# Kernel tuning notes

Hardware: AMD Instinct MI355X
Metric: run time of the kernel (lower is better)

The kernel has to match this reference:

```python
import jax, jax.numpy as jnp
import numpy as np

N_PER_GRAPH = 1000   # nodes per graph block (shape of A)
N_GRAPHS = 100       # number of block-diagonal replicas
N = N_PER_GRAPH * N_GRAPHS  # total nodes = 100000
HIDDEN = 128
DEG = 8
E = N * DEG          # total edges = 800000
LN_EPS = 1e-5


def setup_inputs() -> dict:
    key = jax.random.key(0)
    kx, kr, kc, kw, kb = jax.random.split(key, 5)
    # x rows: [S(N); I(N); R(N); params(N)] with beta in col0, gamma in col1
    x = jax.random.normal(kx, (4 * N, HIDDEN), dtype=jnp.float32)
    # block-diagonal COO edges: indices within each graph offset by graph id * n
    offs = jnp.repeat(jnp.arange(N_GRAPHS, dtype=jnp.int64) * N_PER_GRAPH,
                      N_PER_GRAPH * DEG)
    edge_row = offs + jax.random.randint(kr, (E,), 0, N_PER_GRAPH, dtype=jnp.int64)
    edge_col = offs + jax.random.randint(kc, (E,), 0, N_PER_GRAPH, dtype=jnp.int64)
    W = jax.random.normal(kw, (HIDDEN, HIDDEN), dtype=jnp.float32)
    b = jax.random.normal(kb, (HIDDEN,), dtype=jnp.float32)
    ln_w = jnp.ones((HIDDEN,), dtype=jnp.float32)
    ln_b = jnp.zeros((HIDDEN,), dtype=jnp.float32)
    t = jax.random.uniform(jax.random.fold_in(key, 7), (1,), dtype=jnp.float32)
    return {"t": t, "x": x, "edge_row": edge_row, "edge_col": edge_col,
            "W": W, "b": b, "ln_w": ln_w, "ln_b": ln_b}


def reference(t, x, edge_row, edge_col, W, b, ln_w, ln_b):
    n4 = x.shape[0]
    n = n4 // 4
    sir = x[: 3 * n]                       # [3N, H]
    beta = x[3 * n :, 0]                   # [N]
    gam = x[3 * n :, 1]                    # [N]
    h = jax.nn.relu(sir @ W.T + b)         # Linear + ReLU
    S, I, R = h[:n], h[n : 2 * n], h[2 * n :]
    # block-diagonal adjacency aggregation: AI[row] += I[col]
    AI = jax.ops.segment_sum(I[edge_col], edge_row, num_segments=n)
    dS = -beta[:, None] * (AI * S)
    dI = -dS - gam[:, None] * I
    dR = gam[:, None] * I

    def ln(v):
        m = jnp.mean(v, axis=-1, keepdims=True)
        var = jnp.mean(jnp.square(v - m), axis=-1, keepdims=True)
        return (v - m) * jax.lax.rsqrt(var + LN_EPS) * ln_w + ln_b

    return jnp.concatenate([ln(dS), ln(dI), ln(dR), x[3 * n :]], axis=0)
```

## Files before the change

kernel.cpp:

```cpp
#include <hip/hip_runtime.h>

#define HID 128
#define NPG 1000
#define NGRAPH 100
#define NNODES (NPG * NGRAPH)
#define DEG 8
#define LN_EPS 1e-5f

#define K1_ROWS 128

typedef _Float16 half8 __attribute__((ext_vector_type(8)));
typedef float f32x4 __attribute__((ext_vector_type(4)));

__device__ inline void cvt_split(const float4 a, const float4 b,
                                 half8& hi, half8& lo)
{
    float v[8] = {a.x, a.y, a.z, a.w, b.x, b.y, b.z, b.w};
    #pragma unroll
    for (int i = 0; i < 8; ++i) {
        _Float16 h = (_Float16)v[i];
        hi[i] = h;
        lo[i] = (_Float16)(v[i] - (float)h);
    }
}

__global__ __launch_bounds__(256, 2) void k_gemm_relu(
    const float* __restrict__ x, const float* __restrict__ W,
    const float* __restrict__ bias, float* __restrict__ outS,
    float* __restrict__ outI, int nrows)
{
    __shared__ alignas(16) _Float16 Xh[K1_ROWS * 64];
    __shared__ alignas(16) _Float16 Xl[K1_ROWS * 64];
    __shared__ alignas(16) _Float16 Wh[HID * 64];
    __shared__ alignas(16) _Float16 Wl[HID * 64];

    const int tid  = threadIdx.x;
    const int lane = tid & 63;
    const int w    = tid >> 6;
    const int wr   = (w >> 1) * 64;
    const int wc   = (w & 1) * 64;
    const int r0   = blockIdx.x * K1_ROWS;

    f32x4 acc[4][4];
    #pragma unroll
    for (int i = 0; i < 4; ++i)
        #pragma unroll
        for (int j = 0; j < 4; ++j)
            acc[i][j] = (f32x4){0.f, 0.f, 0.f, 0.f};

    const int l15 = lane & 15;
    const int lg  = lane >> 4;
    const int swz = (lane & 7) << 3;

    for (int kh = 0; kh < 2; ++kh) {
        if (kh) __syncthreads();

        #pragma unroll
        for (int it = 0; it < 4; ++it) {
            int chunk = tid + it * 256;
            int row = chunk >> 3, kg = chunk & 7;
            const float* gp = &x[(size_t)(r0 + row) * HID + kh * 64 + kg * 8];
            float4 a = reinterpret_cast<const float4*>(gp)[0];
            float4 b = reinterpret_cast<const float4*>(gp)[1];
            half8 hi, lo; cvt_split(a, b, hi, lo);
            int widx = (row * 64 + kg * 8) ^ ((row & 7) << 3);
            *reinterpret_cast<half8*>(&Xh[widx]) = hi;
            *reinterpret_cast<half8*>(&Xl[widx]) = lo;
        }
        #pragma unroll
        for (int it = 0; it < 4; ++it) {
            int chunk = tid + it * 256;
            int row = chunk >> 3, kg = chunk & 7;
            const float* gp = &W[(size_t)row * HID + kh * 64 + kg * 8];
            float4 a = reinterpret_cast<const float4*>(gp)[0];
            float4 b = reinterpret_cast<const float4*>(gp)[1];
            half8 hi, lo; cvt_split(a, b, hi, lo);
            int widx = (row * 64 + kg * 8) ^ ((row & 7) << 3);
            *reinterpret_cast<half8*>(&Wh[widx]) = hi;
            *reinterpret_cast<half8*>(&Wl[widx]) = lo;
        }
        __syncthreads();

        #pragma unroll
        for (int kb = 0; kb < 2; ++kb) {
            half8 ah[4], al[4], bh[4], bl[4];
            #pragma unroll
            for (int t = 0; t < 4; ++t) {
                int arow = wr + t * 16 + l15;
                int aidx = (arow * 64 + kb * 32 + lg * 8) ^ swz;
                ah[t] = *reinterpret_cast<const half8*>(&Xh[aidx]);
                al[t] = *reinterpret_cast<const half8*>(&Xl[aidx]);
                int bcol = wc + t * 16 + l15;
                int bidx = (bcol * 64 + kb * 32 + lg * 8) ^ swz;
                bh[t] = *reinterpret_cast<const half8*>(&Wh[bidx]);
                bl[t] = *reinterpret_cast<const half8*>(&Wl[bidx]);
            }
            #pragma unroll
            for (int rt = 0; rt < 4; ++rt)
                #pragma unroll
                for (int ct = 0; ct < 4; ++ct) {
                    acc[rt][ct] = __builtin_amdgcn_mfma_f32_16x16x32_f16(
                        ah[rt], bh[ct], acc[rt][ct], 0, 0, 0);
                    acc[rt][ct] = __builtin_amdgcn_mfma_f32_16x16x32_f16(
                        al[rt], bh[ct], acc[rt][ct], 0, 0, 0);
                    acc[rt][ct] = __builtin_amdgcn_mfma_f32_16x16x32_f16(
                        ah[rt], bl[ct], acc[rt][ct], 0, 0, 0);
                }
        }
    }

    float bc[4];
    #pragma unroll
    for (int ct = 0; ct < 4; ++ct) bc[ct] = bias[wc + ct * 16 + l15];

    #pragma unroll
    for (int rt = 0; rt < 4; ++rt) {
        int rowb = r0 + wr + rt * 16 + lg * 4;
        #pragma unroll
        for (int j = 0; j < 4; ++j) {
            int r = rowb + j;
            if (r < nrows) {
                float* base = (r < NNODES)
                                  ? &outS[(size_t)r * HID]
                                  : &outI[(size_t)(r - NNODES) * HID];
                float* hp = base + wc + l15;
                #pragma unroll
                for (int ct = 0; ct < 4; ++ct)
                    hp[ct * 16] = fmaxf(acc[rt][ct][j] + bc[ct], 0.f);
            }
        }
    }
}

#define BPG  8
#define RPB  (NPG / BPG)
#define ECAP 1280

__global__ __launch_bounds__(256) void k_agg_final(
    const float* __restrict__ x, const float* __restrict__ Sbuf,
    const float* __restrict__ Ibuf, const int* __restrict__ erow,
    const int* __restrict__ ecol, const float* __restrict__ lnw,
    const float* __restrict__ lnb, float* __restrict__ out)
{
    __shared__ int cnt[RPB];
    __shared__ int wp[RPB];
    __shared__ int scan[256];
    __shared__ int cols[ECAP];

    const int g     = blockIdx.x / BPG;
    const int q     = blockIdx.x % BPG;
    const int row0  = q * RPB;
    const int nbase = g * NPG;
    const int ebase = g * (NPG * DEG);
    const int tid   = threadIdx.x;

    if (tid < RPB) cnt[tid] = 0;
    __syncthreads();

    for (int e = tid; e < NPG * DEG; e += 256) {
        int rl = erow[ebase + e] - nbase - row0;
        if ((unsigned)rl < (unsigned)RPB) atomicAdd(&cnt[rl], 1);
    }
    __syncthreads();

    int v = (tid < RPB) ? cnt[tid] : 0;
    scan[tid] = v;
    __syncthreads();
    #pragma unroll
    for (int s = 1; s < 256; s <<= 1) {
        int t = (tid >= s) ? scan[tid - s] : 0;
        __syncthreads();
        scan[tid] += t;
        __syncthreads();
    }
    if (tid < RPB) wp[tid] = scan[tid] - cnt[tid];
    __syncthreads();

    for (int e = tid; e < NPG * DEG; e += 256) {
        int rl = erow[ebase + e] - nbase - row0;
        if ((unsigned)rl < (unsigned)RPB) {
            int p = atomicAdd(&wp[rl], 1);
            if (p < ECAP) cols[p] = ecol[ebase + e];
        }
    }
    __syncthreads();

    const int wave = tid >> 6, lane = tid & 63;
    const int c = lane * 2;
    const size_t N = NNODES;

    const float2 lw = *reinterpret_cast<const float2*>(&lnw[c]);
    const float2 lb = *reinterpret_cast<const float2*>(&lnb[c]);

    auto ln_store = [&](float2 vv, float* dst) {
        float s = vv.x + vv.y;
        #pragma unroll
        for (int m = 1; m < 64; m <<= 1) s += __shfl_xor(s, m);
        const float mean = s * (1.f / 128.f);
        const float dx = vv.x - mean, dy = vv.y - mean;
        float qq = dx * dx + dy * dy;
        #pragma unroll
        for (int m = 1; m < 64; m <<= 1) qq += __shfl_xor(qq, m);
        const float rs = rsqrtf(qq * (1.f / 128.f) + LN_EPS);
        float2 o;
        o.x = dx * rs * lw.x + lb.x;
        o.y = dy * rs * lw.y + lb.y;
        *reinterpret_cast<float2*>(dst) = o;
    };

    for (int n = wave; n < RPB; n += 4) {
        const size_t gn = (size_t)(nbase + row0 + n);

        float2 Sv = *reinterpret_cast<const float2*>(&Sbuf[gn * HID + c]);
        float2 Iv = *reinterpret_cast<const float2*>(&Ibuf[gn * HID + c]);
        float2 T  = *reinterpret_cast<const float2*>(&x[(3 * N + gn) * HID + c]);

        int deg = cnt[n];
        int end = wp[n];
        int j   = end - deg;
        float ax = 0.f, ay = 0.f;
        for (; j + 4 <= end; j += 4) {
            int c0 = cols[j], c1 = cols[j + 1], c2 = cols[j + 2], c3 = cols[j + 3];
            float2 v0 = *reinterpret_cast<const float2*>(&Ibuf[(size_t)c0 * HID + c]);
            float2 v1 = *reinterpret_cast<const float2*>(&Ibuf[(size_t)c1 * HID + c]);
            float2 v2 = *reinterpret_cast<const float2*>(&Ibuf[(size_t)c2 * HID + c]);
            float2 v3 = *reinterpret_cast<const float2*>(&Ibuf[(size_t)c3 * HID + c]);
            ax += v0.x + v1.x + v2.x + v3.x;
            ay += v0.y + v1.y + v2.y + v3.y;
        }
        for (; j < end; j++) {
            float2 v0 = *reinterpret_cast<const float2*>(&Ibuf[(size_t)cols[j] * HID + c]);
            ax += v0.x; ay += v0.y;
        }

        const float beta = __shfl(T.x, 0);
        const float gam  = __shfl(T.y, 0);

        float2 dS, dI, dR;
        dS.x = -beta * (ax * Sv.x);
        dS.y = -beta * (ay * Sv.y);
        dI.x = -dS.x - gam * Iv.x;
        dI.y = -dS.y - gam * Iv.y;
        dR.x = gam * Iv.x;
        dR.y = gam * Iv.y;

        ln_store(dS, &out[gn * HID + c]);
        ln_store(dI, &out[(N + gn) * HID + c]);
        ln_store(dR, &out[(2 * N + gn) * HID + c]);
        *reinterpret_cast<float2*>(&out[(3 * N + gn) * HID + c]) = T;
    }
}

__global__ __launch_bounds__(256) void k_aggregate(
    const float* __restrict__ I, const int* __restrict__ erow,
    const int* __restrict__ ecol, float* __restrict__ AI)
{
    __shared__ int cnt[RPB];
    __shared__ int wp[RPB];
    __shared__ int scan[256];
    __shared__ int cols[ECAP];

    const int g     = blockIdx.x / BPG;
    const int q     = blockIdx.x % BPG;
    const int row0  = q * RPB;
    const int nbase = g * NPG;
    const int ebase = g * (NPG * DEG);
    const int tid   = threadIdx.x;

    if (tid < RPB) cnt[tid] = 0;
    __syncthreads();

    for (int e = tid; e < NPG * DEG; e += 256) {
        int rl = erow[ebase + e] - nbase - row0;
        if ((unsigned)rl < (unsigned)RPB) atomicAdd(&cnt[rl], 1);
    }
    __syncthreads();

    int v = (tid < RPB) ? cnt[tid] : 0;
    scan[tid] = v;
    __syncthreads();
    #pragma unroll
    for (int s = 1; s < 256; s <<= 1) {
        int t = (tid >= s) ? scan[tid - s] : 0;
        __syncthreads();
        scan[tid] += t;
        __syncthreads();
    }
    if (tid < RPB) wp[tid] = scan[tid] - cnt[tid];
    __syncthreads();

    for (int e = tid; e < NPG * DEG; e += 256) {
        int rl = erow[ebase + e] - nbase - row0;
        if ((unsigned)rl < (unsigned)RPB) {
            int p = atomicAdd(&wp[rl], 1);
            if (p < ECAP) cols[p] = ecol[ebase + e];
        }
    }
    __syncthreads();

    const int wave = tid >> 6, lane = tid & 63;
    const int c = lane * 2;
    for (int n = wave; n < RPB; n += 4) {
        int deg = cnt[n];
        int end = wp[n];
        int j   = end - deg;
        float ax = 0.f, ay = 0.f;
        for (; j + 4 <= end; j += 4) {
            int c0 = cols[j], c1 = cols[j + 1], c2 = cols[j + 2], c3 = cols[j + 3];
            float2 v0 = *reinterpret_cast<const float2*>(&I[(size_t)c0 * HID + c]);
            float2 v1 = *reinterpret_cast<const float2*>(&I[(size_t)c1 * HID + c]);
            float2 v2 = *reinterpret_cast<const float2*>(&I[(size_t)c2 * HID + c]);
            float2 v3 = *reinterpret_cast<const float2*>(&I[(size_t)c3 * HID + c]);
            ax += v0.x + v1.x + v2.x + v3.x;
            ay += v0.y + v1.y + v2.y + v3.y;
        }
        for (; j < end; j++) {
            float2 v0 = *reinterpret_cast<const float2*>(&I[(size_t)cols[j] * HID + c]);
            ax += v0.x; ay += v0.y;
        }
        float2 o; o.x = ax; o.y = ay;
        *reinterpret_cast<float2*>(&AI[(size_t)(nbase + row0 + n) * HID + c]) = o;
    }
}

__global__ __launch_bounds__(256) void k_final(
    const float* __restrict__ x, const float* __restrict__ lnw,
    const float* __restrict__ lnb, float* __restrict__ out)
{
    const int wave = threadIdx.x >> 6;
    const int lane = threadIdx.x & 63;
    const size_t i = (size_t)blockIdx.x * 4 + wave;
    const int c    = lane * 2;
    const size_t N = NNODES;

    float2 S  = *reinterpret_cast<const float2*>(&out[i * HID + c]);
    float2 I2 = *reinterpret_cast<const float2*>(&out[(N + i) * HID + c]);
    float2 A  = *reinterpret_cast<const float2*>(&out[(2 * N + i) * HID + c]);

    const float beta = x[(3 * N + i) * HID + 0];
    const float gam  = x[(3 * N + i) * HID + 1];

    float2 dS, dI, dR;
    dS.x = -beta * (A.x * S.x);
    dS.y = -beta * (A.y * S.y);
    dI.x = -dS.x - gam * I2.x;
    dI.y = -dS.y - gam * I2.y;
    dR.x = gam * I2.x;
    dR.y = gam * I2.y;

    const float2 lw = *reinterpret_cast<const float2*>(&lnw[c]);
    const float2 lb = *reinterpret_cast<const float2*>(&lnb[c]);

    auto ln_store = [&](float2 v, float* dst) {
        float s = v.x + v.y;
        #pragma unroll
        for (int m = 1; m < 64; m <<= 1) s += __shfl_xor(s, m);
        const float mean = s * (1.f / 128.f);
        const float dx = v.x - mean, dy = v.y - mean;
        float q = dx * dx + dy * dy;
        #pragma unroll
        for (int m = 1; m < 64; m <<= 1) q += __shfl_xor(q, m);
        const float rs = rsqrtf(q * (1.f / 128.f) + LN_EPS);
        float2 o;
        o.x = dx * rs * lw.x + lb.x;
        o.y = dy * rs * lw.y + lb.y;
        *reinterpret_cast<float2*>(dst) = o;
    };

    ln_store(dS, &out[i * HID + c]);
    ln_store(dI, &out[(N + i) * HID + c]);
    ln_store(dR, &out[(2 * N + i) * HID + c]);

    const float2 t2 =
        *reinterpret_cast<const float2*>(&x[(3 * N + i) * HID + c]);
    *reinterpret_cast<float2*>(&out[(3 * N + i) * HID + c]) = t2;
}

extern "C" void kernel_launch(void* const* d_in, const int* in_sizes, int n_in,
                              void* d_out, int out_size, void* d_ws,
                              size_t ws_size, hipStream_t stream)
{
    const float* x   = (const float*)d_in[1];
    const int* erow  = (const int*)d_in[2];
    const int* ecol  = (const int*)d_in[3];
    const float* W   = (const float*)d_in[4];
    const float* b   = (const float*)d_in[5];
    const float* lnw = (const float*)d_in[6];
    const float* lnb = (const float*)d_in[7];
    float* out = (float*)d_out;

    const int nrows = 2 * NNODES;
    const size_t ineed = (size_t)NNODES * HID * sizeof(float);

    if (d_ws != nullptr && ws_size >= ineed) {
        float* Iws = (float*)d_ws;
        k_gemm_relu<<<(nrows + K1_ROWS - 1) / K1_ROWS, 256, 0, stream>>>(
            x, W, b, out, Iws, nrows);
        k_agg_final<<<NGRAPH * BPG, 256, 0, stream>>>(
            x, out, Iws, erow, ecol, lnw, lnb, out);
    } else {
        float* Iptr  = out + (size_t)NNODES * HID;
        float* AIptr = out + (size_t)2 * NNODES * HID;
        k_gemm_relu<<<(nrows + K1_ROWS - 1) / K1_ROWS, 256, 0, stream>>>(
            x, W, b, out, Iptr, nrows);
        k_aggregate<<<NGRAPH * BPG, 256, 0, stream>>>(Iptr, erow, ecol, AIptr);
        k_final<<<NNODES / 4, 256, 0, stream>>>(x, lnw, lnb, out);
    }
}
```

Measured before the change: 493.9 us.

## Split aggregation into smaller blocks, use float4 half-wave rows, single-pass layernorm

Each graph now maps to 20 blocks of 50 rows instead of 8 blocks of 125, which raises the block count to 2000. Block IDs are remapped in a swizzled order and launch bounds request higher occupancy. Each half-wave handles one row with float4 loads, so two rows run per wave, and layernorm computes sum and sum of squares in one shuffle pass. The cost is that every block rescans the full graph's edge list, so edge reads go up. The one-pass variance is also less numerically stable.

```diff
diff --git a/kernel.cpp b/kernel.cpp
--- a/kernel.cpp
+++ b/kernel.cpp
@@ -132,124 +132,143 @@
     }
 }
 
-#define BPG  8
-#define RPB  (NPG / BPG)
-#define ECAP 1280
-
-__global__ __launch_bounds__(256) void k_agg_final(
+#define BPG2  20
+#define RPB2  50
+#define ECAP2 640
+
+__global__ __launch_bounds__(256, 8) void k_agg_final(
     const float* __restrict__ x, const float* __restrict__ Sbuf,
     const float* __restrict__ Ibuf, const int* __restrict__ erow,
     const int* __restrict__ ecol, const float* __restrict__ lnw,
     const float* __restrict__ lnb, float* __restrict__ out)
 {
-    __shared__ int cnt[RPB];
-    __shared__ int wp[RPB];
-    __shared__ int scan[256];
-    __shared__ int cols[ECAP];
-
-    const int g     = blockIdx.x / BPG;
-    const int q     = blockIdx.x % BPG;
-    const int row0  = q * RPB;
+    __shared__ int cnt[RPB2];
+    __shared__ int wp[RPB2];
+    __shared__ int scn[64];
+    __shared__ int cols[ECAP2];
+
+    const int bi    = blockIdx.x;
+    const int id    = (bi & 7) * (NGRAPH * BPG2 / 8) + (bi >> 3);
+    const int g     = id / BPG2;
+    const int q     = id % BPG2;
+    const int row0  = q * RPB2;
     const int nbase = g * NPG;
     const int ebase = g * (NPG * DEG);
     const int tid   = threadIdx.x;
 
-    if (tid < RPB) cnt[tid] = 0;
+    if (tid < RPB2) cnt[tid] = 0;
     __syncthreads();
 
     for (int e = tid; e < NPG * DEG; e += 256) {
         int rl = erow[ebase + e] - nbase - row0;
-        if ((unsigned)rl < (unsigned)RPB) atomicAdd(&cnt[rl], 1);
-    }
-    __syncthreads();
-
-    int v = (tid < RPB) ? cnt[tid] : 0;
-    scan[tid] = v;
-    __syncthreads();
-    #pragma unroll
-    for (int s = 1; s < 256; s <<= 1) {
-        int t = (tid >= s) ? scan[tid - s] : 0;
+        if ((unsigned)rl < (unsigned)RPB2) atomicAdd(&cnt[rl], 1);
+    }
+    __syncthreads();
+
+    if (tid < 64) scn[tid] = (tid < RPB2) ? cnt[tid] : 0;
+    __syncthreads();
+    #pragma unroll
+    for (int s = 1; s < 64; s <<= 1) {
+        int t = (tid < 64 && tid >= s) ? scn[tid - s] : 0;
         __syncthreads();
-        scan[tid] += t;
+        if (tid < 64) scn[tid] += t;
         __syncthreads();
     }
-    if (tid < RPB) wp[tid] = scan[tid] - cnt[tid];
+    if (tid < RPB2) wp[tid] = scn[tid] - cnt[tid];
     __syncthreads();
 
     for (int e = tid; e < NPG * DEG; e += 256) {
         int rl = erow[ebase + e] - nbase - row0;
-        if ((unsigned)rl < (unsigned)RPB) {
+        if ((unsigned)rl < (unsigned)RPB2) {
             int p = atomicAdd(&wp[rl], 1);
-            if (p < ECAP) cols[p] = ecol[ebase + e];
+            if (p < ECAP2) cols[p] = ecol[ebase + e];
         }
     }
     __syncthreads();
 
     const int wave = tid >> 6, lane = tid & 63;
-    const int c = lane * 2;
+    const int h    = lane >> 5;
+    const int l32  = lane & 31;
+    const int c4   = l32 * 4;
     const size_t N = NNODES;
 
-    const float2 lw = *reinterpret_cast<const float2*>(&lnw[c]);
-    const float2 lb = *reinterpret_cast<const float2*>(&lnb[c]);
-
-    auto ln_store = [&](float2 vv, float* dst) {
-        float s = vv.x + vv.y;
-        #pragma unroll
-        for (int m = 1; m < 64; m <<= 1) s += __shfl_xor(s, m);
+    const float4 lwv = *reinterpret_cast<const float4*>(&lnw[c4]);
+    const float4 lbv = *reinterpret_cast<const float4*>(&lnb[c4]);
+
+    auto ln_store = [&](float4 v, float* dst) {
+        float s  = v.x + v.y + v.z + v.w;
+        float qq = v.x * v.x + v.y * v.y + v.z * v.z + v.w * v.w;
+        #pragma unroll
+        for (int m = 1; m < 32; m <<= 1) {
+            s  += __shfl_xor(s, m);
+            qq += __shfl_xor(qq, m);
+        }
         const float mean = s * (1.f / 128.f);
-        const float dx = vv.x - mean, dy = vv.y - mean;
-        float qq = dx * dx + dy * dy;
-        #pragma unroll
-        for (int m = 1; m < 64; m <<= 1) qq += __shfl_xor(qq, m);
-        const float rs = rsqrtf(qq * (1.f / 128.f) + LN_EPS);
-        float2 o;
-        o.x = dx * rs * lw.x + lb.x;
-        o.y = dy * rs * lw.y + lb.y;
-        *reinterpret_cast<float2*>(dst) = o;
+        const float var  = fmaxf(qq * (1.f / 128.f) - mean * mean, 0.f);
+        const float rs   = rsqrtf(var + LN_EPS);
+        float4 o;
+        o.x = (v.x - mean) * rs * lwv.x + lbv.x;
+        o.y = (v.y - mean) * rs * lwv.y + lbv.y;
+        o.z = (v.z - mean) * rs * lwv.z + lbv.z;
+        o.w = (v.w - mean) * rs * lwv.w + lbv.w;
+        *reinterpret_cast<float4*>(dst) = o;
     };
 
-    for (int n = wave; n < RPB; n += 4) {
+    for (int n0 = wave * 2; n0 < RPB2; n0 += 8) {
+        const int n = n0 + h;
         const size_t gn = (size_t)(nbase + row0 + n);
 
-        float2 Sv = *reinterpret_cast<const float2*>(&Sbuf[gn * HID + c]);
-        float2 Iv = *reinterpret_cast<const float2*>(&Ibuf[gn * HID + c]);
-        float2 T  = *reinterpret_cast<const float2*>(&x[(3 * N + gn) * HID + c]);
+        float4 Sv = *reinterpret_cast<const float4*>(&Sbuf[gn * HID + c4]);
+        float4 Iv = *reinterpret_cast<const float4*>(&Ibuf[gn * HID + c4]);
+        float4 T  = *reinterpret_cast<const float4*>(&x[(3 * N + gn) * HID + c4]);
 
         int deg = cnt[n];
         int end = wp[n];
         int j   = end - deg;
-        float ax = 0.f, ay = 0.f;
+        float ax = 0.f, ay = 0.f, az = 0.f, aw = 0.f;
         for (; j + 4 <= end; j += 4) {
             int c0 = cols[j], c1 = cols[j + 1], c2 = cols[j + 2], c3 = cols[j + 3];
-            float2 v0 = *reinterpret_cast<const float2*>(&Ibuf[(size_t)c0 * HID + c]);
-            float2 v1 = *reinterpret_cast<const float2*>(&Ibuf[(size_t)c1 * HID + c]);
-            float2 v2 = *reinterpret_cast<const float2*>(&Ibuf[(size_t)c2 * HID + c]);
-            float2 v3 = *reinterpret_cast<const float2*>(&Ibuf[(size_t)c3 * HID + c]);
+            float4 v0 = *reinterpret_cast<const float4*>(&Ibuf[(size_t)c0 * HID + c4]);
+            float4 v1 = *reinterpret_cast<const float4*>(&Ibuf[(size_t)c1 * HID + c4]);
+            float4 v2 = *reinterpret_cast<const float4*>(&Ibuf[(size_t)c2 * HID + c4]);
+            float4 v3 = *reinterpret_cast<const float4*>(&Ibuf[(size_t)c3 * HID + c4]);
             ax += v0.x + v1.x + v2.x + v3.x;
             ay += v0.y + v1.y + v2.y + v3.y;
+            az += v0.z + v1.z + v2.z + v3.z;
+            aw += v0.w + v1.w + v2.w + v3.w;
         }
         for (; j < end; j++) {
-            float2 v0 = *reinterpret_cast<const float2*>(&Ibuf[(size_t)cols[j] * HID + c]);
-            ax += v0.x; ay += v0.y;
-        }
-
-        const float beta = __shfl(T.x, 0);
-        const float gam  = __shfl(T.y, 0);
-
-        float2 dS, dI, dR;
+            float4 v0 = *reinterpret_cast<const float4*>(&Ibuf[(size_t)cols[j] * HID + c4]);
+            ax += v0.x; ay += v0.y; az += v0.z; aw += v0.w;
+        }
+
+        const float beta = __shfl(T.x, h << 5);
+        const float gam  = __shfl(T.y, h << 5);
+
+        float4 dS, dI, dR;
         dS.x = -beta * (ax * Sv.x);
         dS.y = -beta * (ay * Sv.y);
+        dS.z = -beta * (az * Sv.z);
+        dS.w = -beta * (aw * Sv.w);
         dI.x = -dS.x - gam * Iv.x;
         dI.y = -dS.y - gam * Iv.y;
+        dI.z = -dS.z - gam * Iv.z;
+        dI.w = -dS.w - gam * Iv.w;
         dR.x = gam * Iv.x;
         dR.y = gam * Iv.y;
-
-        ln_store(dS, &out[gn * HID + c]);
-        ln_store(dI, &out[(N + gn) * HID + c]);
-        ln_store(dR, &out[(2 * N + gn) * HID + c]);
-        *reinterpret_cast<float2*>(&out[(3 * N + gn) * HID + c]) = T;
-    }
-}
+        dR.z = gam * Iv.z;
+        dR.w = gam * Iv.w;
+
+        ln_store(dS, &out[gn * HID + c4]);
+        ln_store(dI, &out[(N + gn) * HID + c4]);
+        ln_store(dR, &out[(2 * N + gn) * HID + c4]);
+        *reinterpret_cast<float4*>(&out[(3 * N + gn) * HID + c4]) = T;
+    }
+}
+
+#define BPG  8
+#define RPB  (NPG / BPG)
+#define ECAP 1280
 
 __global__ __launch_bounds__(256) void k_aggregate(
     const float* __restrict__ I, const int* __restrict__ erow,
@@ -396,7 +415,7 @@
         float* Iws = (float*)d_ws;
         k_gemm_relu<<<(nrows + K1_ROWS - 1) / K1_ROWS, 256, 0, stream>>>(
             x, W, b, out, Iws, nrows);
-        k_agg_final<<<NGRAPH * BPG, 256, 0, stream>>>(
+        k_agg_final<<<NGRAPH * BPG2, 256, 0, stream>>>(
             x, out, Iws, erow, ecol, lnw, lnb, out);
     } else {
         float* Iptr  = out + (size_t)NNODES * HID;
```

Result: faster. 460.1 us (-6.9%).
